# Kernel optimization log

Hardware: AMD Instinct MI355X
Metric: run time of the kernel (lower is better)

Reference implementation:

```python
import jax, jax.numpy as jnp
import numpy as np

H = 8  # num heads (init_kwargs)

def setup_inputs() -> dict:
    key = jax.random.key(0)
    ks = jax.random.split(key, 12)
    B, L, D = 2, 256, 512
    dk = D // H
    s = 0.02
    return {
        "query": jax.random.normal(ks[0], (B, L, D), jnp.float32),
        "key": jax.random.normal(ks[1], (B, L, D), jnp.float32),
        "value": jax.random.normal(ks[2], (B, L, D), jnp.float32),
        "mask": jnp.ones((B, L, L), jnp.int32),
        "relative_q": jax.random.normal(ks[3], (B * H, L, L, dk), jnp.float32) * s,
        "relative_v": jax.random.normal(ks[4], (B * H, L, L, dk), jnp.float32) * s,
        "Wq": jax.random.normal(ks[5], (D, D), jnp.float32) * s,
        "bq": jnp.zeros((D,), jnp.float32),
        "Wk": jax.random.normal(ks[6], (D, D), jnp.float32) * s,
        "bk": jnp.zeros((D,), jnp.float32),
        "Wv": jax.random.normal(ks[7], (D, D), jnp.float32) * s,
        "bv": jnp.zeros((D,), jnp.float32),
        "Wo": jax.random.normal(ks[8], (D, D), jnp.float32) * s,
        "bo": jnp.zeros((D,), jnp.float32),
    }


def reference(query, key, value, mask, relative_q, relative_v,
              Wq, bq, Wk, bk, Wv, bv, Wo, bo):
    B, L, D = query.shape
    dk = D // H
    scale = 1.0 / jnp.sqrt(jnp.asarray(dk, query.dtype))

    def proj(x, W, b):
        # torch Linear: x @ W^T + b, then split heads -> [B*H, L, dk]
        y = jnp.einsum('bld,ed->ble', x, W) + b
        return y.reshape(B, L, H, dk).transpose(0, 2, 1, 3).reshape(B * H, L, dk)

    q = proj(query, Wq, bq)
    k = proj(key, Wk, bk)
    v = proj(value, Wv, bv)

    # scores [B*H, L, L]
    scores = jnp.einsum('bid,bjd->bij', q, k) * scale
    # relative_q bias: q_i . rel_q[i, j] per (batch*head)
    scores = scores + jnp.einsum('bid,bijd->bij', q, relative_q)

    mask_bh = jnp.repeat(mask[:, None], H, axis=1).reshape(B * H, L, L)
    neg = jnp.asarray(-1e9, scores.dtype)
    scores = jnp.where(mask_bh == 0, neg, scores)

    p = jax.nn.softmax(scores, axis=-1)  # dropout is identity at eval

    ctx = jnp.einsum('bij,bjd->bid', p, v)
    ctx = ctx + jnp.einsum('bij,bijd->bid', p, relative_v)

    ctx = ctx.reshape(B, H, L, dk).transpose(0, 2, 1, 3).reshape(B, L, D)
    return jnp.einsum('bld,ed->ble', ctx, Wo) + bo
```

## Files before the change

### kernel.cpp

```cpp
#include <hip/hip_runtime.h>
#include <hip/hip_bf16.h>

#define L_SEQ 256
#define D_MODEL 512
#define N_HEADS 8
#define DK 64
#define N_BATCH 2
#define BH (N_BATCH * N_HEADS)

__global__ __launch_bounds__(256) void gemm_nt(
    const float* __restrict__ X, const float* __restrict__ W,
    const float* __restrict__ bias, float* __restrict__ out, int split_heads)
{
    __shared__ float Xs[32][33];
    __shared__ float Ws[32][33];

    const int tid  = threadIdx.x;
    const int row0 = blockIdx.x * 32;
    const int col0 = blockIdx.y * 32;
    const int tx = tid & 31;
    const int ty = tid >> 5;

    float acc0 = 0.f, acc1 = 0.f, acc2 = 0.f, acc3 = 0.f;

    const int lr = tid >> 3;
    const int lc = (tid & 7) << 2;

    for (int k0 = 0; k0 < 512; k0 += 32) {
        float4 xv = *(const float4*)&X[(size_t)(row0 + lr) * 512 + k0 + lc];
        float4 wv = *(const float4*)&W[(size_t)(col0 + lr) * 512 + k0 + lc];
        Xs[lr][lc + 0] = xv.x; Xs[lr][lc + 1] = xv.y;
        Xs[lr][lc + 2] = xv.z; Xs[lr][lc + 3] = xv.w;
        Ws[lr][lc + 0] = wv.x; Ws[lr][lc + 1] = wv.y;
        Ws[lr][lc + 2] = wv.z; Ws[lr][lc + 3] = wv.w;
        __syncthreads();
#pragma unroll
        for (int kk = 0; kk < 32; ++kk) {
            float w = Ws[tx][kk];
            acc0 += Xs[ty][kk] * w;
            acc1 += Xs[ty + 8][kk] * w;
            acc2 += Xs[ty + 16][kk] * w;
            acc3 += Xs[ty + 24][kk] * w;
        }
        __syncthreads();
    }

    const int c = col0 + tx;
    const float bv = bias[c];
    float accs[4] = {acc0, acc1, acc2, acc3};
#pragma unroll
    for (int r = 0; r < 4; ++r) {
        const int row = row0 + ty + r * 8;
        const float val = accs[r] + bv;
        if (split_heads) {
            const int b = row >> 8, l = row & 255;
            const int h = c >> 6,  d = c & 63;
            out[(size_t)((b * N_HEADS + h) * L_SEQ + l) * DK + d] = val;
        } else {
            out[(size_t)row * 512 + c] = val;
        }
    }
}

__global__ __launch_bounds__(256) void attn_rel(
    const float* __restrict__ q, const float* __restrict__ k,
    const float* __restrict__ v, const int* __restrict__ mask,
    const float* __restrict__ relq, const float* __restrict__ relv,
    float* __restrict__ ctx)
{
    const int bh = blockIdx.x >> 8;
    const int i  = blockIdx.x & 255;
    const int b  = bh >> 3;
    const int h  = bh & 7;

    const int t    = threadIdx.x;
    const int lane = t & 63;
    const int wave = t >> 6;

    __shared__ float q_s[64];
    __shared__ float sc[256];
    __shared__ float red[8];
    __shared__ float ctxp[4][64];

    const float scale = 0.125f;

    if (t < 64) q_s[t] = q[(size_t)(bh * L_SEQ + i) * DK + t];
    __syncthreads();

    const int jgrp = t >> 4;
    const int d0   = (t & 15) << 2;

    const float q0 = q_s[d0], q1 = q_s[d0 + 1], q2 = q_s[d0 + 2], q3 = q_s[d0 + 3];

    const float* relq_row = relq + ((size_t)bh * L_SEQ + i) * L_SEQ * DK;
    const float* k_bh = k + (size_t)bh * L_SEQ * DK;
    const int* mask_row = mask + (size_t)(b * L_SEQ + i) * L_SEQ;

#pragma unroll 4
    for (int p = 0; p < 16; ++p) {
        const int j = p * 16 + jgrp;
        float4 rq = *(const float4*)&relq_row[(size_t)j * DK + d0];
        float4 kk = *(const float4*)&k_bh[(size_t)j * DK + d0];
        float s = q0 * fmaf(scale, kk.x, rq.x)
                + q1 * fmaf(scale, kk.y, rq.y)
                + q2 * fmaf(scale, kk.z, rq.z)
                + q3 * fmaf(scale, kk.w, rq.w);
        s += __shfl_xor(s, 1);
        s += __shfl_xor(s, 2);
        s += __shfl_xor(s, 4);
        s += __shfl_xor(s, 8);
        if ((t & 15) == 0) {
            const int m = mask_row[j];
            sc[j] = (m == 0) ? -1e9f : s;
        }
    }
    __syncthreads();

    const float s_own = sc[t];
    float mval = s_own;
#pragma unroll
    for (int o = 32; o >= 1; o >>= 1) mval = fmaxf(mval, __shfl_xor(mval, o));
    if (lane == 0) red[wave] = mval;
    __syncthreads();
    mval = fmaxf(fmaxf(red[0], red[1]), fmaxf(red[2], red[3]));

    const float e = __expf(s_own - mval);
    float ssum = e;
#pragma unroll
    for (int o = 32; o >= 1; o >>= 1) ssum += __shfl_xor(ssum, o);
    if (lane == 0) red[4 + wave] = ssum;
    __syncthreads();
    ssum = red[4] + red[5] + red[6] + red[7];

    sc[t] = e / ssum;
    __syncthreads();

    const float* relv_row = relv + ((size_t)bh * L_SEQ + i) * L_SEQ * DK;
    const float* v_bh = v + (size_t)bh * L_SEQ * DK;

    float a0 = 0.f, a1 = 0.f, a2 = 0.f, a3 = 0.f;
#pragma unroll 4
    for (int p = 0; p < 16; ++p) {
        const int j = p * 16 + jgrp;
        float4 rv = *(const float4*)&relv_row[(size_t)j * DK + d0];
        float4 vv = *(const float4*)&v_bh[(size_t)j * DK + d0];
        const float pw = sc[j];
        a0 = fmaf(pw, vv.x + rv.x, a0);
        a1 = fmaf(pw, vv.y + rv.y, a1);
        a2 = fmaf(pw, vv.z + rv.z, a2);
        a3 = fmaf(pw, vv.w + rv.w, a3);
    }
    a0 += __shfl_xor(a0, 16); a0 += __shfl_xor(a0, 32);
    a1 += __shfl_xor(a1, 16); a1 += __shfl_xor(a1, 32);
    a2 += __shfl_xor(a2, 16); a2 += __shfl_xor(a2, 32);
    a3 += __shfl_xor(a3, 16); a3 += __shfl_xor(a3, 32);
    if (lane < 16) {
        ctxp[wave][lane * 4 + 0] = a0;
        ctxp[wave][lane * 4 + 1] = a1;
        ctxp[wave][lane * 4 + 2] = a2;
        ctxp[wave][lane * 4 + 3] = a3;
    }
    __syncthreads();

    if (t < 64) {
        const float r = ctxp[0][t] + ctxp[1][t] + ctxp[2][t] + ctxp[3][t];
        ctx[(size_t)(b * L_SEQ + i) * D_MODEL + h * DK + t] = r;
    }
}

extern "C" void kernel_launch(void* const* d_in, const int* in_sizes, int n_in,
                              void* d_out, int out_size, void* d_ws, size_t ws_size,
                              hipStream_t stream) {
    const float* query = (const float*)d_in[0];
    const float* key   = (const float*)d_in[1];
    const float* value = (const float*)d_in[2];
    const int*   mask  = (const int*)d_in[3];
    const float* relq  = (const float*)d_in[4];
    const float* relv  = (const float*)d_in[5];
    const float* Wq = (const float*)d_in[6];
    const float* bq = (const float*)d_in[7];
    const float* Wk = (const float*)d_in[8];
    const float* bk = (const float*)d_in[9];
    const float* Wv = (const float*)d_in[10];
    const float* bv = (const float*)d_in[11];
    const float* Wo = (const float*)d_in[12];
    const float* bo = (const float*)d_in[13];
    float* out = (float*)d_out;

    float* ws = (float*)d_ws;
    const size_t QKV = (size_t)BH * L_SEQ * DK;
    float* q_ws   = ws;
    float* k_ws   = ws + QKV;
    float* v_ws   = ws + 2 * QKV;
    float* ctx_ws = ws + 3 * QKV;

    dim3 gg(16, 16, 1);
    gemm_nt<<<gg, 256, 0, stream>>>(query, Wq, bq, q_ws, 1);
    gemm_nt<<<gg, 256, 0, stream>>>(key,   Wk, bk, k_ws, 1);
    gemm_nt<<<gg, 256, 0, stream>>>(value, Wv, bv, v_ws, 1);

    attn_rel<<<BH * L_SEQ, 256, 0, stream>>>(q_ws, k_ws, v_ws, mask, relq, relv, ctx_ws);

    gemm_nt<<<gg, 256, 0, stream>>>(ctx_ws, Wo, bo, out, 0);
}
```

Before: 657.2 us.

## Split QK and PV dense parts into tiled GEMMs, batch QKV projections

Moves the q·k score term and the p·v context term out of the per-row attention kernel into separate shared-memory-tiled GEMM kernels. The main attention kernel now streams only relative_q and relative_v plus precomputed scores, and writes probabilities to workspace. The three input projections run in a single launch over blockIdx.z, and the GEMM uses a 2x2 register tile with float4 shared-memory reads. This adds launches and extra workspace traffic for the score and probability matrices, while the dominant relq/relv streaming cost stays the same.

```diff
diff --git a/kernel.cpp b/kernel.cpp
--- a/kernel.cpp
+++ b/kernel.cpp
@@ -8,65 +8,123 @@
 #define N_BATCH 2
 #define BH (N_BATCH * N_HEADS)
 
-__global__ __launch_bounds__(256) void gemm_nt(
-    const float* __restrict__ X, const float* __restrict__ W,
-    const float* __restrict__ bias, float* __restrict__ out, int split_heads)
+__global__ __launch_bounds__(256) void proj_gemm(
+    const float* __restrict__ X0, const float* __restrict__ X1, const float* __restrict__ X2,
+    const float* __restrict__ W0, const float* __restrict__ W1, const float* __restrict__ W2,
+    const float* __restrict__ B0, const float* __restrict__ B1, const float* __restrict__ B2,
+    float* __restrict__ O0, float* __restrict__ O1, float* __restrict__ O2,
+    int split_heads)
 {
-    __shared__ float Xs[32][33];
-    __shared__ float Ws[32][33];
-
-    const int tid  = threadIdx.x;
+    const int z = blockIdx.z;
+    const float* X    = (z == 0) ? X0 : (z == 1) ? X1 : X2;
+    const float* W    = (z == 0) ? W0 : (z == 1) ? W1 : W2;
+    const float* bias = (z == 0) ? B0 : (z == 1) ? B1 : B2;
+    float* out        = (z == 0) ? O0 : (z == 1) ? O1 : O2;
+
+    __shared__ float Xs[32][36];
+    __shared__ float Ws[32][36];
+
+    const int t = threadIdx.x;
     const int row0 = blockIdx.x * 32;
     const int col0 = blockIdx.y * 32;
-    const int tx = tid & 31;
-    const int ty = tid >> 5;
-
-    float acc0 = 0.f, acc1 = 0.f, acc2 = 0.f, acc3 = 0.f;
-
-    const int lr = tid >> 3;
-    const int lc = (tid & 7) << 2;
+    const int lr = t >> 3;
+    const int lc = (t & 7) << 2;
+    const int r0 = (t >> 4) * 2;
+    const int c0 = (t & 15) * 2;
+
+    float a00 = 0.f, a01 = 0.f, a10 = 0.f, a11 = 0.f;
 
     for (int k0 = 0; k0 < 512; k0 += 32) {
-        float4 xv = *(const float4*)&X[(size_t)(row0 + lr) * 512 + k0 + lc];
-        float4 wv = *(const float4*)&W[(size_t)(col0 + lr) * 512 + k0 + lc];
-        Xs[lr][lc + 0] = xv.x; Xs[lr][lc + 1] = xv.y;
-        Xs[lr][lc + 2] = xv.z; Xs[lr][lc + 3] = xv.w;
-        Ws[lr][lc + 0] = wv.x; Ws[lr][lc + 1] = wv.y;
-        Ws[lr][lc + 2] = wv.z; Ws[lr][lc + 3] = wv.w;
         __syncthreads();
-#pragma unroll
-        for (int kk = 0; kk < 32; ++kk) {
-            float w = Ws[tx][kk];
-            acc0 += Xs[ty][kk] * w;
-            acc1 += Xs[ty + 8][kk] * w;
-            acc2 += Xs[ty + 16][kk] * w;
-            acc3 += Xs[ty + 24][kk] * w;
-        }
+        *(float4*)&Xs[lr][lc] = *(const float4*)&X[(size_t)(row0 + lr) * 512 + k0 + lc];
+        *(float4*)&Ws[lr][lc] = *(const float4*)&W[(size_t)(col0 + lr) * 512 + k0 + lc];
         __syncthreads();
-    }
-
-    const int c = col0 + tx;
-    const float bv = bias[c];
-    float accs[4] = {acc0, acc1, acc2, acc3};
-#pragma unroll
-    for (int r = 0; r < 4; ++r) {
-        const int row = row0 + ty + r * 8;
-        const float val = accs[r] + bv;
-        if (split_heads) {
-            const int b = row >> 8, l = row & 255;
-            const int h = c >> 6,  d = c & 63;
-            out[(size_t)((b * N_HEADS + h) * L_SEQ + l) * DK + d] = val;
-        } else {
-            out[(size_t)row * 512 + c] = val;
-        }
-    }
+#pragma unroll
+        for (int kk = 0; kk < 32; kk += 4) {
+            const float4 x0 = *(const float4*)&Xs[r0][kk];
+            const float4 x1 = *(const float4*)&Xs[r0 + 1][kk];
+            const float4 w0 = *(const float4*)&Ws[c0][kk];
+            const float4 w1 = *(const float4*)&Ws[c0 + 1][kk];
+            a00 = fmaf(x0.x, w0.x, fmaf(x0.y, w0.y, fmaf(x0.z, w0.z, fmaf(x0.w, w0.w, a00))));
+            a01 = fmaf(x0.x, w1.x, fmaf(x0.y, w1.y, fmaf(x0.z, w1.z, fmaf(x0.w, w1.w, a01))));
+            a10 = fmaf(x1.x, w0.x, fmaf(x1.y, w0.y, fmaf(x1.z, w0.z, fmaf(x1.w, w0.w, a10))));
+            a11 = fmaf(x1.x, w1.x, fmaf(x1.y, w1.y, fmaf(x1.z, w1.z, fmaf(x1.w, w1.w, a11))));
+        }
+    }
+
+    const float accs[2][2] = {{a00, a01}, {a10, a11}};
+#pragma unroll
+    for (int dr = 0; dr < 2; ++dr) {
+#pragma unroll
+        for (int dc = 0; dc < 2; ++dc) {
+            const int row = row0 + r0 + dr;
+            const int c   = col0 + c0 + dc;
+            const float val = accs[dr][dc] + bias[c];
+            if (split_heads) {
+                const int b = row >> 8, l = row & 255;
+                const int h = c >> 6,  d = c & 63;
+                out[(size_t)((b * N_HEADS + h) * L_SEQ + l) * DK + d] = val;
+            } else {
+                out[(size_t)row * 512 + c] = val;
+            }
+        }
+    }
+}
+
+__global__ __launch_bounds__(256) void qk_gemm(
+    const float* __restrict__ q, const float* __restrict__ k,
+    float* __restrict__ s0)
+{
+    __shared__ float Qs[32][68];
+    __shared__ float Ks[32][68];
+
+    const int bh = blockIdx.z;
+    const int i0 = blockIdx.x * 32;
+    const int j0 = blockIdx.y * 32;
+    const int t = threadIdx.x;
+
+    const int lr = t >> 3;
+    const int lc0 = (t & 7) * 8;
+    {
+        const float* qrow = q + ((size_t)(bh * L_SEQ + i0 + lr)) * DK;
+        const float* krow = k + ((size_t)(bh * L_SEQ + j0 + lr)) * DK;
+        *(float4*)&Qs[lr][lc0]     = *(const float4*)&qrow[lc0];
+        *(float4*)&Qs[lr][lc0 + 4] = *(const float4*)&qrow[lc0 + 4];
+        *(float4*)&Ks[lr][lc0]     = *(const float4*)&krow[lc0];
+        *(float4*)&Ks[lr][lc0 + 4] = *(const float4*)&krow[lc0 + 4];
+    }
+    __syncthreads();
+
+    const int r0 = (t >> 4) * 2;
+    const int c0 = (t & 15) * 2;
+    float a00 = 0.f, a01 = 0.f, a10 = 0.f, a11 = 0.f;
+#pragma unroll
+    for (int kk = 0; kk < 64; kk += 4) {
+        const float4 x0 = *(const float4*)&Qs[r0][kk];
+        const float4 x1 = *(const float4*)&Qs[r0 + 1][kk];
+        const float4 w0 = *(const float4*)&Ks[c0][kk];
+        const float4 w1 = *(const float4*)&Ks[c0 + 1][kk];
+        a00 = fmaf(x0.x, w0.x, fmaf(x0.y, w0.y, fmaf(x0.z, w0.z, fmaf(x0.w, w0.w, a00))));
+        a01 = fmaf(x0.x, w1.x, fmaf(x0.y, w1.y, fmaf(x0.z, w1.z, fmaf(x0.w, w1.w, a01))));
+        a10 = fmaf(x1.x, w0.x, fmaf(x1.y, w0.y, fmaf(x1.z, w0.z, fmaf(x1.w, w0.w, a10))));
+        a11 = fmaf(x1.x, w1.x, fmaf(x1.y, w1.y, fmaf(x1.z, w1.z, fmaf(x1.w, w1.w, a11))));
+    }
+
+    const float scale = 0.125f;
+    const float accs[2][2] = {{a00, a01}, {a10, a11}};
+#pragma unroll
+    for (int dr = 0; dr < 2; ++dr)
+#pragma unroll
+        for (int dc = 0; dc < 2; ++dc)
+            s0[((size_t)bh * L_SEQ + i0 + r0 + dr) * L_SEQ + j0 + c0 + dc] =
+                accs[dr][dc] * scale;
 }
 
 __global__ __launch_bounds__(256) void attn_rel(
-    const float* __restrict__ q, const float* __restrict__ k,
-    const float* __restrict__ v, const int* __restrict__ mask,
+    const float* __restrict__ q, const int* __restrict__ mask,
     const float* __restrict__ relq, const float* __restrict__ relv,
-    float* __restrict__ ctx)
+    const float* __restrict__ s0, float* __restrict__ p_out,
+    float* __restrict__ ctxrel)
 {
     const int bh = blockIdx.x >> 8;
     const int i  = blockIdx.x & 255;
@@ -82,9 +140,8 @@
     __shared__ float red[8];
     __shared__ float ctxp[4][64];
 
-    const float scale = 0.125f;
-
     if (t < 64) q_s[t] = q[(size_t)(bh * L_SEQ + i) * DK + t];
+    sc[t] = s0[((size_t)bh * L_SEQ + i) * L_SEQ + t];
     __syncthreads();
 
     const int jgrp = t >> 4;
@@ -93,25 +150,20 @@
     const float q0 = q_s[d0], q1 = q_s[d0 + 1], q2 = q_s[d0 + 2], q3 = q_s[d0 + 3];
 
     const float* relq_row = relq + ((size_t)bh * L_SEQ + i) * L_SEQ * DK;
-    const float* k_bh = k + (size_t)bh * L_SEQ * DK;
     const int* mask_row = mask + (size_t)(b * L_SEQ + i) * L_SEQ;
 
 #pragma unroll 4
     for (int p = 0; p < 16; ++p) {
         const int j = p * 16 + jgrp;
         float4 rq = *(const float4*)&relq_row[(size_t)j * DK + d0];
-        float4 kk = *(const float4*)&k_bh[(size_t)j * DK + d0];
-        float s = q0 * fmaf(scale, kk.x, rq.x)
-                + q1 * fmaf(scale, kk.y, rq.y)
-                + q2 * fmaf(scale, kk.z, rq.z)
-                + q3 * fmaf(scale, kk.w, rq.w);
+        float s = fmaf(q0, rq.x, fmaf(q1, rq.y, fmaf(q2, rq.z, q3 * rq.w)));
         s += __shfl_xor(s, 1);
         s += __shfl_xor(s, 2);
         s += __shfl_xor(s, 4);
         s += __shfl_xor(s, 8);
         if ((t & 15) == 0) {
             const int m = mask_row[j];
-            sc[j] = (m == 0) ? -1e9f : s;
+            sc[j] = (m == 0) ? -1e9f : (sc[j] + s);
         }
     }
     __syncthreads();
@@ -132,23 +184,23 @@
     __syncthreads();
     ssum = red[4] + red[5] + red[6] + red[7];
 
-    sc[t] = e / ssum;
+    const float pfin = e / ssum;
+    sc[t] = pfin;
+    p_out[((size_t)bh * L_SEQ + i) * L_SEQ + t] = pfin;
     __syncthreads();
 
     const float* relv_row = relv + ((size_t)bh * L_SEQ + i) * L_SEQ * DK;
-    const float* v_bh = v + (size_t)bh * L_SEQ * DK;
 
     float a0 = 0.f, a1 = 0.f, a2 = 0.f, a3 = 0.f;
 #pragma unroll 4
     for (int p = 0; p < 16; ++p) {
         const int j = p * 16 + jgrp;
         float4 rv = *(const float4*)&relv_row[(size_t)j * DK + d0];
-        float4 vv = *(const float4*)&v_bh[(size_t)j * DK + d0];
         const float pw = sc[j];
-        a0 = fmaf(pw, vv.x + rv.x, a0);
-        a1 = fmaf(pw, vv.y + rv.y, a1);
-        a2 = fmaf(pw, vv.z + rv.z, a2);
-        a3 = fmaf(pw, vv.w + rv.w, a3);
+        a0 = fmaf(pw, rv.x, a0);
+        a1 = fmaf(pw, rv.y, a1);
+        a2 = fmaf(pw, rv.z, a2);
+        a3 = fmaf(pw, rv.w, a3);
     }
     a0 += __shfl_xor(a0, 16); a0 += __shfl_xor(a0, 32);
     a1 += __shfl_xor(a1, 16); a1 += __shfl_xor(a1, 32);
@@ -164,7 +216,72 @@
 
     if (t < 64) {
         const float r = ctxp[0][t] + ctxp[1][t] + ctxp[2][t] + ctxp[3][t];
-        ctx[(size_t)(b * L_SEQ + i) * D_MODEL + h * DK + t] = r;
+        ctxrel[(size_t)(b * L_SEQ + i) * D_MODEL + h * DK + t] = r;
+    }
+}
+
+__global__ __launch_bounds__(256) void pv_gemm(
+    const float* __restrict__ P, const float* __restrict__ V,
+    const float* __restrict__ ctxrel, float* __restrict__ ctx)
+{
+    __shared__ float Ps[32][260];
+    __shared__ float Vs[64][68];
+
+    const int bh = blockIdx.y;
+    const int i0 = blockIdx.x * 32;
+    const int b = bh >> 3, h = bh & 7;
+    const int t = threadIdx.x;
+
+    {
+        const int lr  = t >> 3;
+        const int lc0 = (t & 7) * 4;
+        const float* prow = P + ((size_t)(bh * L_SEQ + i0 + lr)) * L_SEQ;
+#pragma unroll
+        for (int qq = 0; qq < 8; ++qq)
+            *(float4*)&Ps[lr][lc0 + 32 * qq] = *(const float4*)&prow[lc0 + 32 * qq];
+    }
+
+    const int r0 = (t >> 4) * 2;
+    const int c0 = (t & 15) * 4;
+
+    float4 acc0 = {0.f, 0.f, 0.f, 0.f};
+    float4 acc1 = {0.f, 0.f, 0.f, 0.f};
+
+    for (int j0 = 0; j0 < 256; j0 += 64) {
+        __syncthreads();
+        {
+            const int lr  = t >> 2;
+            const int lc0 = (t & 3) * 4;
+            const float* vrow = V + ((size_t)(bh * L_SEQ + j0 + lr)) * DK;
+#pragma unroll
+            for (int qq = 0; qq < 4; ++qq)
+                *(float4*)&Vs[lr][lc0 + 16 * qq] = *(const float4*)&vrow[lc0 + 16 * qq];
+        }
+        __syncthreads();
+#pragma unroll 8
+        for (int jj = 0; jj < 64; ++jj) {
+            const float4 vv = *(const float4*)&Vs[jj][c0];
+            const float p0 = Ps[r0][j0 + jj];
+            const float p1 = Ps[r0 + 1][j0 + jj];
+            acc0.x = fmaf(p0, vv.x, acc0.x);
+            acc0.y = fmaf(p0, vv.y, acc0.y);
+            acc0.z = fmaf(p0, vv.z, acc0.z);
+            acc0.w = fmaf(p0, vv.w, acc0.w);
+            acc1.x = fmaf(p1, vv.x, acc1.x);
+            acc1.y = fmaf(p1, vv.y, acc1.y);
+            acc1.z = fmaf(p1, vv.z, acc1.z);
+            acc1.w = fmaf(p1, vv.w, acc1.w);
+        }
+    }
+
+#pragma unroll
+    for (int dr = 0; dr < 2; ++dr) {
+        const size_t base = ((size_t)(b * L_SEQ + i0 + r0 + dr)) * D_MODEL + h * DK + c0;
+        const float4 rel = *(const float4*)&ctxrel[base];
+        const float4 a = dr ? acc1 : acc0;
+        float4 o;
+        o.x = a.x + rel.x; o.y = a.y + rel.y; o.z = a.z + rel.z; o.w = a.w + rel.w;
+        *(float4*)&ctx[base] = o;
     }
 }
 
@@ -189,17 +306,25 @@
 
     float* ws = (float*)d_ws;
     const size_t QKV = (size_t)BH * L_SEQ * DK;
-    float* q_ws   = ws;
-    float* k_ws   = ws + QKV;
-    float* v_ws   = ws + 2 * QKV;
-    float* ctx_ws = ws + 3 * QKV;
-
-    dim3 gg(16, 16, 1);
-    gemm_nt<<<gg, 256, 0, stream>>>(query, Wq, bq, q_ws, 1);
-    gemm_nt<<<gg, 256, 0, stream>>>(key,   Wk, bk, k_ws, 1);
-    gemm_nt<<<gg, 256, 0, stream>>>(value, Wv, bv, v_ws, 1);
-
-    attn_rel<<<BH * L_SEQ, 256, 0, stream>>>(q_ws, k_ws, v_ws, mask, relq, relv, ctx_ws);
-
-    gemm_nt<<<gg, 256, 0, stream>>>(ctx_ws, Wo, bo, out, 0);
-}
+    const size_t SSZ = (size_t)BH * L_SEQ * L_SEQ;
+    float* q_ws      = ws;
+    float* k_ws      = ws + QKV;
+    float* v_ws      = ws + 2 * QKV;
+    float* s0_ws     = ws + 3 * QKV;
+    float* p_ws      = s0_ws + SSZ;
+    float* ctxrel_ws = p_ws + SSZ;
+    float* ctx_ws    = ctxrel_ws + QKV;
+
+    proj_gemm<<<dim3(16, 16, 3), 256, 0, stream>>>(
+        query, key, value, Wq, Wk, Wv, bq, bk, bv, q_ws, k_ws, v_ws, 1);
+
+    qk_gemm<<<dim3(8, 8, BH), 256, 0, stream>>>(q_ws, k_ws, s0_ws);
+
+    attn_rel<<<BH * L_SEQ, 256, 0, stream>>>(q_ws, mask, relq, relv,
+                                             s0_ws, p_ws, ctxrel_ws);
+
+    pv_gemm<<<dim3(8, BH), 256, 0, stream>>>(p_ws, v_ws, ctxrel_ws, ctx_ws);
+
+    proj_gemm<<<dim3(16, 16, 1), 256, 0, stream>>>(
+        ctx_ws, ctx_ws, ctx_ws, Wo, Wo, Wo, bo, bo, bo, out, out, out, 0);
+}
```

New measurement: 597.2 us. 9.1% less time.
